# Optimization experiments

Measured on AMD Instinct MI355X. Metric: run time of the kernel, lower is better.

Reference implementation:

```python
import jax, jax.numpy as jnp
import numpy as np

N_HEAD = 16
N_KV_HEAD = 4
HEAD_DIM = 128
N_EMBD = 2048
ROPE_BASE = 100000.0
EPS = 1e-6
MASK_VAL = -10000.0


def _rope_tables(t, dtype):
    half = HEAD_DIM // 2
    inv_freq = 1.0 / (ROPE_BASE ** (jnp.arange(half, dtype=jnp.float32) / half))
    freqs = jnp.arange(t, dtype=jnp.float32)[:, None] * inv_freq[None, :]  # [t, half]
    return jnp.cos(freqs).astype(dtype), jnp.sin(freqs).astype(dtype)


def _apply_rope(x, cos, sin):
    # x: [b, t, h, d]; cos/sin: [t, d//2]
    x1, x2 = jnp.split(x, 2, axis=-1)
    c = cos[None, :, None, :]
    s = sin[None, :, None, :]
    return jnp.concatenate([x1 * c + x2 * s, -x1 * s + x2 * c], axis=-1)


def _rms_norm(x):
    return x * jax.lax.rsqrt(jnp.mean(jnp.square(x), axis=-1, keepdims=True) + EPS)


def setup_inputs() -> dict:
    key = jax.random.key(0)
    ks = jax.random.split(key, 5)
    b, t = 2, 2048
    std = 0.02
    return {
        "x": jax.random.normal(ks[0], (b, t, N_EMBD), dtype=jnp.float32),
        "wq": jax.random.normal(ks[1], (N_EMBD, N_HEAD * HEAD_DIM), dtype=jnp.float32) * std,
        "wk": jax.random.normal(ks[2], (N_EMBD, N_KV_HEAD * HEAD_DIM), dtype=jnp.float32) * std,
        "wv": jax.random.normal(ks[3], (N_EMBD, N_KV_HEAD * HEAD_DIM), dtype=jnp.float32) * std,
        "wo": jax.random.normal(ks[4], (N_EMBD, N_EMBD), dtype=jnp.float32) * std,
    }


def reference(x, wq, wk, wv, wo):
    b, t, _ = x.shape
    group = N_HEAD // N_KV_HEAD

    q = (x @ wq).reshape(b, t, N_HEAD, HEAD_DIM)
    k = (x @ wk).reshape(b, t, N_KV_HEAD, HEAD_DIM)
    v = (x @ wv).reshape(b, t, N_KV_HEAD, HEAD_DIM)

    cos, sin = _rope_tables(t, x.dtype)
    q = _rms_norm(_apply_rope(q, cos, sin))
    k = _rms_norm(_apply_rope(k, cos, sin))

    # GQA expand: [b,t,kvh,d] -> [b,t,h,d]
    k = jnp.repeat(k, group, axis=2)
    v = jnp.repeat(v, group, axis=2)

    scale = jax.lax.rsqrt(jnp.asarray(HEAD_DIM, dtype=q.dtype))
    scores = jnp.einsum("bqhd,bkhd->bhqk", q, k) * scale  # [b,h,t,t]

    causal = jnp.tril(jnp.ones((t, t), dtype=bool))
    scores = jnp.where(causal[None, None, :, :], scores, jnp.asarray(MASK_VAL, scores.dtype))

    probs = jax.nn.softmax(scores.astype(jnp.float32), axis=-1).astype(scores.dtype)

    y = jnp.einsum("bhqk,bkhd->bqhd", probs, v).reshape(b, t, N_EMBD)
    return y @ wo
```

## Files before the change

kernel.cpp:

```cpp
#include <hip/hip_runtime.h>
#include <stdint.h>

typedef unsigned short u16;
typedef unsigned int   u32;
typedef float f32x4  __attribute__((ext_vector_type(4)));
typedef float f32x16 __attribute__((ext_vector_type(16)));
typedef short s16x8  __attribute__((ext_vector_type(8)));

#define T_SEQ 2048
#define NE    2048
#define NH    16
#define NKV   4
#define HD    128
#define QKVW  3072

__device__ __forceinline__ u16 f2bf(float f){
  u32 u = __float_as_uint(f);
  u32 r = u + 0x7FFFu + ((u >> 16) & 1u);
  return (u16)(r >> 16);
}
__device__ __forceinline__ float bf2f(u16 h){ return __uint_as_float(((u32)h) << 16); }

__device__ __forceinline__ u32 pkbf(float a, float b){
  u32 r; asm("v_cvt_pk_bf16_f32 %0, %1, %2" : "=v"(r) : "v"(a), "v"(b)); return r;
}

typedef __attribute__((address_space(3))) u32 lds_u32;
typedef __attribute__((address_space(1))) u32 glb_u32;
__device__ __forceinline__ void g2lds16(const void* g, void* l){
  __builtin_amdgcn_global_load_lds((const glb_u32*)g, (lds_u32*)l, 16, 0, 0);
}

#define PREP_NBLK 18944
__global__ __launch_bounds__(256) void k_prep(const float* __restrict__ x,
                                              const float* __restrict__ wq, const float* __restrict__ wk,
                                              const float* __restrict__ wv, const float* __restrict__ wo,
                                              u16* __restrict__ xb, u16* __restrict__ wqkvT, u16* __restrict__ woT,
                                              float* __restrict__ cosT, float* __restrict__ sinT){
  __shared__ float t[32][33];
  const int blk = blockIdx.x, tid = threadIdx.x;
  if (blk < 8192){
    int i = (blk * 256 + tid) * 4;
    float4 v = *(const float4*)(x + i);
    ushort4 o; o.x = f2bf(v.x); o.y = f2bf(v.y); o.z = f2bf(v.z); o.w = f2bf(v.w);
    *(ushort4*)(xb + i) = o;
    return;
  }
  if (blk >= 18432){
    int i = (blk - 18432) * 256 + tid;
    int tt = i >> 6, j = i & 63;
    float inv = expf(-(float)j * (11.512925464970229f / 64.0f));
    float f = (float)tt * inv;
    cosT[i] = cosf(f);
    sinT[i] = sinf(f);
    return;
  }
  const float* in; u16* out; int C; int tt;
  if      (blk < 12288){ in = wq; out = wqkvT;                     C = 2048; tt = blk - 8192;  }
  else if (blk < 13312){ in = wk; out = wqkvT + (size_t)2048*2048; C = 512;  tt = blk - 12288; }
  else if (blk < 14336){ in = wv; out = wqkvT + (size_t)2560*2048; C = 512;  tt = blk - 13312; }
  else                 { in = wo; out = woT;                       C = 2048; tt = blk - 14336; }
  const int r0 = (tt & 63) * 32, c0 = (tt >> 6) * 32;
  const int tx = tid & 31, ty = tid >> 5;
  #pragma unroll
  for (int i = 0; i < 4; ++i) t[ty + i*8][tx] = in[(size_t)(r0 + ty + i*8) * C + c0 + tx];
  __syncthreads();
  #pragma unroll
  for (int i = 0; i < 4; ++i) out[(size_t)(c0 + ty + i*8) * 2048 + r0 + tx] = f2bf(t[tx][ty + i*8]);
}

#define POST_NBLK 22528
__global__ __launch_bounds__(256) void k_post(u16* __restrict__ qkv, u16* __restrict__ vtb,
                                              const float* __restrict__ cosT, const float* __restrict__ sinT,
                                              float qscale){
  __shared__ u16 tsh[32][33];
  const int blk = blockIdx.x, tid = threadIdx.x;
  if (blk < 20480){
    u16* base; int log2h; float scale; int rh;
    if (blk < 16384){ base = qkv;        log2h = 4; scale = qscale; rh = blk * 4 + (tid >> 6); }
    else            { base = qkv + 2048; log2h = 2; scale = 1.0f;   rh = (blk - 16384) * 4 + (tid >> 6); }
    const int lane = tid & 63;
    const int row = rh >> log2h;
    const int h   = rh & ((1 << log2h) - 1);
    const int t   = row & (T_SEQ - 1);
    u16* p = base + (size_t)row * QKVW + h * HD;
    float x1 = bf2f(p[lane]), x2 = bf2f(p[lane + 64]);
    float c = cosT[t * 64 + lane], s = sinT[t * 64 + lane];
    float y1 = x1 * c + x2 * s;
    float y2 = x2 * c - x1 * s;
    float sq = y1 * y1 + y2 * y2;
    #pragma unroll
    for (int off = 32; off; off >>= 1) sq += __shfl_xor(sq, off);
    float sc = rsqrtf(sq * (1.0f / 128.0f) + 1e-6f) * scale;
    p[lane]      = f2bf(y1 * sc);
    p[lane + 64] = f2bf(y2 * sc);
    return;
  }
  const int tt = blk - 20480;
  const int r0 = (tt & 63) * 32, c0 = ((tt >> 6) & 15) * 32, b = tt >> 10;
  const u16* ib = qkv + (size_t)b * T_SEQ * QKVW + 2560;
  u16*       ob = vtb + (size_t)b * 512 * T_SEQ;
  const int tx = tid & 31, ty = tid >> 5;
  #pragma unroll
  for (int i = 0; i < 4; ++i) tsh[ty + i*8][tx] = ib[(size_t)(r0 + ty + i*8) * QKVW + c0 + tx];
  __syncthreads();
  #pragma unroll
  for (int i = 0; i < 4; ++i) ob[(size_t)(c0 + ty + i*8) * T_SEQ + r0 + tx] = tsh[tx][ty + i*8];
}

__device__ __forceinline__ void cstore(u16* C, size_t i, float v){ C[i] = f2bf(v); }
__device__ __forceinline__ void cstore(float* C, size_t i, float v){ C[i] = v; }

__device__ __forceinline__ void stage_half(const u16* __restrict__ G, int row0, int K, int k0,
                                           u16* lds, int w, int lane){
  #pragma unroll
  for (int call = 0; call < 2; ++call){
    const int o  = call * 256 + w * 64 + lane;
    const int rp = o >> 3, sl = o & 7;
    const int lg = sl ^ (rp & 7);
    const int row = rp * 2 + (lg >> 2);
    const int kc  = lg & 3;
    g2lds16(G + (size_t)(row0 + row) * K + k0 + kc * 8, lds + (size_t)(call * 256 + w * 64) * 8);
  }
}

__device__ __forceinline__ s16x8 ldsFrag(const u16* slotBase, int row, int kchunk){
  const int byte = (row >> 1) * 128 + (((((row & 1) << 2) | kchunk) ^ ((row >> 1) & 7)) << 4);
  return *(const s16x8*)((const char*)slotBase + byte);
}

template <typename CT>
__global__ __launch_bounds__(256, 3) void k_gemm(const u16* __restrict__ A, const u16* __restrict__ BT,
                                                 CT* __restrict__ C, int M, int N, int K, int NPX){
  __shared__ u16 As[3 * 4096];
  __shared__ u16 Bs[3 * 4096];
  const int tid  = threadIdx.x;
  const int lane = tid & 63;
  const int w    = tid >> 6;
  const int wr = w >> 1, wc = w & 1;
  const int bid = blockIdx.x;
  const int xcd = bid & 7, ii = bid >> 3;
  const int ntile = xcd * NPX + ii % NPX;
  const int mtile = ii / NPX;
  const int tm0 = mtile * 128, tn0 = ntile * 128;
  const int frow = lane & 15, fk = lane >> 4;

  f32x4 acc[4][4] = {};
  const int nkt = K >> 6;

  stage_half(A,  tm0, K, 0,  As,        w, lane);
  stage_half(BT, tn0, K, 0,  Bs,        w, lane);
  stage_half(A,  tm0, K, 32, As + 4096, w, lane);
  stage_half(BT, tn0, K, 32, Bs + 4096, w, lane);
  asm volatile("s_waitcnt vmcnt(4)" ::: "memory");
  __builtin_amdgcn_s_barrier();

  int s = 0;
  #pragma unroll 1
  for (int t = 0; t < nkt; ++t){
    const int s1 = (s + 1 > 2) ? 0 : s + 1;
    const int s2 = (s + 2 > 2) ? s - 1 : s + 2;
    const bool more = (t + 1 < nkt);

    if (more){
      stage_half(A,  tm0, K, (t + 1) * 64,  As + s2 * 4096, w, lane);
      stage_half(BT, tn0, K, (t + 1) * 64,  Bs + s2 * 4096, w, lane);
    }
    {
      const u16* Ap = As + s * 4096;
      const u16* Bp = Bs + s * 4096;
      s16x8 af[4], bfr[4];
      #pragma unroll
      for (int m = 0; m < 4; ++m) af[m]  = ldsFrag(Ap, wr * 64 + m * 16 + frow, fk);
      #pragma unroll
      for (int n = 0; n < 4; ++n) bfr[n] = ldsFrag(Bp, wc * 64 + n * 16 + frow, fk);
      __builtin_amdgcn_s_setprio(1);
      #pragma unroll
      for (int m = 0; m < 4; ++m)
        #pragma unroll
        for (int n = 0; n < 4; ++n)
          acc[m][n] = __builtin_amdgcn_mfma_f32_16x16x32_bf16(af[m], bfr[n], acc[m][n], 0, 0, 0);
      __builtin_amdgcn_s_setprio(0);
    }
    if (more) asm volatile("s_waitcnt vmcnt(4)" ::: "memory");
    else      asm volatile("s_waitcnt vmcnt(0)" ::: "memory");
    __builtin_amdgcn_s_barrier();

    if (more){
      stage_half(A,  tm0, K, (t + 1) * 64 + 32, As + s * 4096, w, lane);
      stage_half(BT, tn0, K, (t + 1) * 64 + 32, Bs + s * 4096, w, lane);
    }
    {
      const u16* Ap = As + s1 * 4096;
      const u16* Bp = Bs + s1 * 4096;
      s16x8 af[4], bfr[4];
      #pragma unroll
      for (int m = 0; m < 4; ++m) af[m]  = ldsFrag(Ap, wr * 64 + m * 16 + frow, fk);
      #pragma unroll
      for (int n = 0; n < 4; ++n) bfr[n] = ldsFrag(Bp, wc * 64 + n * 16 + frow, fk);
      __builtin_amdgcn_s_setprio(1);
      #pragma unroll
      for (int m = 0; m < 4; ++m)
        #pragma unroll
        for (int n = 0; n < 4; ++n)
          acc[m][n] = __builtin_amdgcn_mfma_f32_16x16x32_bf16(af[m], bfr[n], acc[m][n], 0, 0, 0);
      __builtin_amdgcn_s_setprio(0);
    }
    if (more){
      asm volatile("s_waitcnt vmcnt(4)" ::: "memory");
      __builtin_amdgcn_s_barrier();
    }
    s = s2;
  }

  #pragma unroll
  for (int m = 0; m < 4; ++m){
    const int row0 = tm0 + wr * 64 + m * 16 + ((lane >> 4) << 2);
    #pragma unroll
    for (int n = 0; n < 4; ++n){
      const int col = tn0 + wc * 64 + n * 16 + (lane & 15);
      #pragma unroll
      for (int r = 0; r < 4; ++r)
        cstore(C, (size_t)(row0 + r) * N + col, acc[m][n][r]);
    }
  }
}

__device__ __forceinline__ s16x8 ldsK(const u16* base, int row, int colB){
  int a = row * 256 + colB; a ^= (row & 7) << 4;
  return *(const s16x8*)((const char*)base + a);
}
__device__ __forceinline__ s16x8 ldsV(const u16* base, int row, int colB){
  int a = row * 128 + colB; a ^= (row & 7) << 4;
  return *(const s16x8*)((const char*)base + a);
}

__global__ __launch_bounds__(256, 2) void k_attn(const u16* __restrict__ qkv, const u16* __restrict__ vt,
                                                 u16* __restrict__ yb){
  __shared__ u16 Kt[2][64 * 128];
  __shared__ u16 Vt[2][128 * 64];
  const int tid = threadIdx.x, lane = tid & 63, w = tid >> 6;
  const int ql = lane & 31, hi = lane >> 5;

  const int bx  = blockIdx.x;
  const int xcd = bx & 7;
  const int b   = xcd >> 2;
  const int kvh = xcd & 3;
  const int slot = bx >> 3;
  const int hl  = slot >> 4;
  const int p   = (slot + 5 * hl) & 15;
  const int h   = kvh * 4 + hl;

  const int tile = (w < 2) ? (31 - p) : p;
  const int tq0  = tile * 64 + (w & 1) * 32;
  const int myq  = tq0 + ql;
  const int nkb  = 32 - p;

  const u16* kg  = qkv + (size_t)(b * T_SEQ) * QKVW + 2048 + kvh * 128;
  const u16* vgb = vt + ((size_t)(b * 512 + kvh * 128)) * T_SEQ;

  auto stageK = [&](int kbI, u16* dst){
    const int ks = kbI * 64;
    #pragma unroll
    for (int cc = 0; cc < 4; ++cc){
      const int call = w * 4 + cc;
      const int o = call * 64 + lane;
      const int f = o ^ ((o >> 4) & 7);
      g2lds16(kg + (size_t)(ks + (o >> 4)) * QKVW + (f & 15) * 8, dst + call * 512);
    }
  };
  auto stageV = [&](int kbI, u16* dst){
    const int ks = kbI * 64;
    #pragma unroll
    for (int cc = 0; cc < 4; ++cc){
      const int call = w * 4 + cc;
      const int o = call * 64 + lane;
      const int f = o ^ ((o >> 3) & 7);
      g2lds16(vgb + (size_t)(o >> 3) * T_SEQ + ks + (f & 7) * 8, dst + call * 512);
    }
  };

  stageK(0, Kt[0]);
  stageV(0, Vt[0]);

  const u16* qrow = qkv + ((size_t)(b * T_SEQ + myq)) * QKVW + h * HD + hi * 8;
  s16x8 qf[8];
  #pragma unroll
  for (int kc = 0; kc < 8; ++kc) qf[kc] = *(const s16x8*)(qrow + kc * 16);

  f32x16 O[4] = {};
  float mloc = -1e30f, lloc = 0.0f;

  asm volatile("s_waitcnt vmcnt(0)" ::: "memory");
  __builtin_amdgcn_s_barrier();

  for (int kbI = 0; kbI < nkb; ++kbI){
    const int ks  = kbI * 64;
    const int cur = kbI & 1;

    if (kbI + 1 < nkb){
      stageV(kbI + 1, Vt[cur ^ 1]);
      stageK(kbI + 1, Kt[cur ^ 1]);
    }

    if (ks <= tq0 + 31){
      const u16* Kc = Kt[cur];
      const u16* Vc = Vt[cur];
      const bool doN1 = (ks + 32 <= tq0 + 31);
      f32x16 S0 = {}, S1 = {};
      __builtin_amdgcn_s_setprio(1);
      #pragma unroll
      for (int kc = 0; kc < 8; ++kc)
        S0 = __builtin_amdgcn_mfma_f32_32x32x16_bf16(ldsK(Kc, ql, kc*32 + hi*16), qf[kc], S0, 0, 0, 0);
      if (doN1){
        #pragma unroll
        for (int kc = 0; kc < 8; ++kc)
          S1 = __builtin_amdgcn_mfma_f32_32x32x16_bf16(ldsK(Kc, 32 + ql, kc*32 + hi*16), qf[kc], S1, 0, 0, 0);
      }
      __builtin_amdgcn_s_setprio(0);
      if (ks + 31 > tq0){
        #pragma unroll
        for (int r = 0; r < 16; ++r)
          if (ks + (r&3) + 8*(r>>2) + 4*hi > myq) S0[r] = -1e30f;
      }
      if (doN1 && (ks + 63 > tq0)){
        #pragma unroll
        for (int r = 0; r < 16; ++r)
          if (ks + 32 + (r&3) + 8*(r>>2) + 4*hi > myq) S1[r] = -1e30f;
      }
      float mr = -1e30f;
      #pragma unroll
      for (int r = 0; r < 16; ++r) mr = fmaxf(mr, S0[r]);
      if (doN1){
        #pragma unroll
        for (int r = 0; r < 16; ++r) mr = fmaxf(mr, S1[r]);
      }
      mr = fmaxf(mr, __shfl_xor(mr, 32));
      if (!__all(mr <= mloc + 8.0f)){
        const float mn = fmaxf(mloc, mr);
        const float a  = __expf(mloc - mn);
        mloc = mn; lloc *= a;
        #pragma unroll
        for (int dt = 0; dt < 4; ++dt)
          #pragma unroll
          for (int r = 0; r < 16; ++r) O[dt][r] *= a;
      }
      float rs = 0.0f;
      #pragma unroll
      for (int r = 0; r < 16; ++r){ S0[r] = __expf(S0[r] - mloc); rs += S0[r]; }
      if (doN1){
        #pragma unroll
        for (int r = 0; r < 16; ++r){ S1[r] = __expf(S1[r] - mloc); rs += S1[r]; }
      }
      rs += __shfl_xor(rs, 32);
      lloc += rs;
      u32 bw[16];
      {
        u32 pk[8], pp[8];
        #pragma unroll
        for (int j = 0; j < 8; ++j) pk[j] = pkbf(S0[2*j], S0[2*j+1]);
        #pragma unroll
        for (int j = 0; j < 8; ++j) pp[j] = (u32)__shfl_xor((int)pk[j], 32);
        bw[0] = hi ? pp[2] : pk[0];  bw[1] = hi ? pp[3] : pk[1];
        bw[2] = hi ? pk[2] : pp[0];  bw[3] = hi ? pk[3] : pp[1];
        bw[4] = hi ? pp[6] : pk[4];  bw[5] = hi ? pp[7] : pk[5];
        bw[6] = hi ? pk[6] : pp[4];  bw[7] = hi ? pk[7] : pp[5];
      }
      int nkc = 2;
      if (doN1){
        u32 pk[8], pp[8];
        #pragma unroll
        for (int j = 0; j < 8; ++j) pk[j] = pkbf(S1[2*j], S1[2*j+1]);
        #pragma unroll
        for (int j = 0; j < 8; ++j) pp[j] = (u32)__shfl_xor((int)pk[j], 32);
        bw[8]  = hi ? pp[2] : pk[0];  bw[9]  = hi ? pp[3] : pk[1];
        bw[10] = hi ? pk[2] : pp[0];  bw[11] = hi ? pk[3] : pp[1];
        bw[12] = hi ? pp[6] : pk[4];  bw[13] = hi ? pp[7] : pk[5];
        bw[14] = hi ? pk[6] : pp[4];  bw[15] = hi ? pk[7] : pp[5];
        nkc = 4;
      }
      __builtin_amdgcn_s_setprio(1);
      #pragma unroll
      for (int kc = 0; kc < 4; ++kc){
        if (kc < nkc){
          union { u32 u[4]; s16x8 v; } pb;
          pb.u[0] = bw[kc*4+0]; pb.u[1] = bw[kc*4+1]; pb.u[2] = bw[kc*4+2]; pb.u[3] = bw[kc*4+3];
          #pragma unroll
          for (int dt = 0; dt < 4; ++dt)
            O[dt] = __builtin_amdgcn_mfma_f32_32x32x16_bf16(ldsV(Vc, dt*32 + ql, kc*32 + hi*16), pb.v, O[dt], 0, 0, 0);
        }
      }
      __builtin_amdgcn_s_setprio(0);
    }

    asm volatile("s_waitcnt vmcnt(0)" ::: "memory");
    __builtin_amdgcn_s_barrier();
  }

  const float linv = 1.0f / lloc;
  u16* yr = yb + ((size_t)(b * T_SEQ + myq)) * NE + h * HD;
  #pragma unroll
  for (int dt = 0; dt < 4; ++dt){
    #pragma unroll
    for (int mq = 0; mq < 4; ++mq){
      uint2 s;
      s.x = pkbf(O[dt][4*mq+0] * linv, O[dt][4*mq+1] * linv);
      s.y = pkbf(O[dt][4*mq+2] * linv, O[dt][4*mq+3] * linv);
      *(uint2*)(yr + dt*32 + 8*mq + 4*hi) = s;
    }
  }
}

extern "C" void kernel_launch(void* const* d_in, const int* in_sizes, int n_in,
                              void* d_out, int out_size, void* d_ws, size_t ws_size,
                              hipStream_t stream){
  const float* x  = (const float*)d_in[0];
  const float* wq = (const float*)d_in[1];
  const float* wk = (const float*)d_in[2];
  const float* wv = (const float*)d_in[3];
  const float* wo = (const float*)d_in[4];
  float* out = (float*)d_out;

  char* w = (char*)d_ws;
  u16* xb    = (u16*)w;  w += (size_t)4096 * 2048 * 2;
  u16* wqkvT = (u16*)w;  w += (size_t)3072 * 2048 * 2;
  u16* woT   = (u16*)w;  w += (size_t)2048 * 2048 * 2;
  u16* qkv   = (u16*)w;  w += (size_t)4096 * 3072 * 2;
  u16* vtb   = (u16*)w;  w += (size_t)4096 * 512  * 2;
  u16* yb    = (u16*)w;  w += (size_t)4096 * 2048 * 2;
  float* cosT = (float*)w; w += (size_t)2048 * 64 * 4;
  float* sinT = (float*)w; w += (size_t)2048 * 64 * 4;

  const float SCALE = 0.08838834764831845f;

  k_prep<<<PREP_NBLK, 256, 0, stream>>>(x, wq, wk, wv, wo, xb, wqkvT, woT, cosT, sinT);

  k_gemm<u16><<<768, 256, 0, stream>>>(xb, wqkvT, qkv, 4096, QKVW, 2048, 3);

  k_post<<<POST_NBLK, 256, 0, stream>>>(qkv, vtb, cosT, sinT, SCALE);

  k_attn<<<512, 256, 0, stream>>>(qkv, vtb, yb);

  k_gemm<float><<<512, 256, 0, stream>>>(yb, woT, out, 4096, 2048, 2048, 2);
}
```

Measured before the change: 220.9 us.

## Widen GEMM tiles to 128x256 with per-wave 128x64 subtiles and remap blocks

The GEMM kernel's block tile grows from 128x128 to 128x256. Each of the four waves now computes a 128x64 strip, holding 8x4 accumulators, and the B staging buffer is doubled. The block-to-tile mapping is also changed so that the four consecutive m-tiles on an XCD share a B column tile, and the grid size is halved for both GEMMs. This raises arithmetic intensity per LDS load and improves L2 reuse, at the cost of more registers (occupancy hint drops from 3 to 2) and fewer blocks, which for the 256-block output GEMM means at most one wave of blocks over the CUs.

```diff
diff --git a/kernel.cpp b/kernel.cpp
--- a/kernel.cpp
+++ b/kernel.cpp
@@ -111,10 +111,11 @@
 __device__ __forceinline__ void cstore(u16* C, size_t i, float v){ C[i] = f2bf(v); }
 __device__ __forceinline__ void cstore(float* C, size_t i, float v){ C[i] = v; }
 
+template <int NCALL>
 __device__ __forceinline__ void stage_half(const u16* __restrict__ G, int row0, int K, int k0,
                                            u16* lds, int w, int lane){
   #pragma unroll
-  for (int call = 0; call < 2; ++call){
+  for (int call = 0; call < NCALL; ++call){
     const int o  = call * 256 + w * 64 + lane;
     const int rp = o >> 3, sl = o & 7;
     const int lg = sl ^ (rp & 7);
@@ -130,29 +131,28 @@
 }
 
 template <typename CT>
-__global__ __launch_bounds__(256, 3) void k_gemm(const u16* __restrict__ A, const u16* __restrict__ BT,
-                                                 CT* __restrict__ C, int M, int N, int K, int NPX){
+__global__ __launch_bounds__(256, 2) void k_gemm(const u16* __restrict__ A, const u16* __restrict__ BT,
+                                                 CT* __restrict__ C, int M, int N, int K){
   __shared__ u16 As[3 * 4096];
-  __shared__ u16 Bs[3 * 4096];
+  __shared__ u16 Bs[3 * 8192];
   const int tid  = threadIdx.x;
   const int lane = tid & 63;
   const int w    = tid >> 6;
-  const int wr = w >> 1, wc = w & 1;
   const int bid = blockIdx.x;
   const int xcd = bid & 7, ii = bid >> 3;
-  const int ntile = xcd * NPX + ii % NPX;
-  const int mtile = ii / NPX;
-  const int tm0 = mtile * 128, tn0 = ntile * 128;
+  const int mtile = xcd * 4 + (ii & 3);
+  const int ntile = ii >> 2;
+  const int tm0 = mtile * 128, tn0 = ntile * 256;
   const int frow = lane & 15, fk = lane >> 4;
 
-  f32x4 acc[4][4] = {};
+  f32x4 acc[8][4] = {};
   const int nkt = K >> 6;
 
-  stage_half(A,  tm0, K, 0,  As,        w, lane);
-  stage_half(BT, tn0, K, 0,  Bs,        w, lane);
-  stage_half(A,  tm0, K, 32, As + 4096, w, lane);
-  stage_half(BT, tn0, K, 32, Bs + 4096, w, lane);
-  asm volatile("s_waitcnt vmcnt(4)" ::: "memory");
+  stage_half<2>(A,  tm0, K, 0,  As,        w, lane);
+  stage_half<4>(BT, tn0, K, 0,  Bs,        w, lane);
+  stage_half<2>(A,  tm0, K, 32, As + 4096, w, lane);
+  stage_half<4>(BT, tn0, K, 32, Bs + 8192, w, lane);
+  asm volatile("s_waitcnt vmcnt(6)" ::: "memory");
   __builtin_amdgcn_s_barrier();
 
   int s = 0;
@@ -163,62 +163,62 @@
     const bool more = (t + 1 < nkt);
 
     if (more){
-      stage_half(A,  tm0, K, (t + 1) * 64,  As + s2 * 4096, w, lane);
-      stage_half(BT, tn0, K, (t + 1) * 64,  Bs + s2 * 4096, w, lane);
+      stage_half<2>(A,  tm0, K, (t + 1) * 64,  As + s2 * 4096, w, lane);
+      stage_half<4>(BT, tn0, K, (t + 1) * 64,  Bs + s2 * 8192, w, lane);
     }
     {
       const u16* Ap = As + s * 4096;
-      const u16* Bp = Bs + s * 4096;
-      s16x8 af[4], bfr[4];
-      #pragma unroll
-      for (int m = 0; m < 4; ++m) af[m]  = ldsFrag(Ap, wr * 64 + m * 16 + frow, fk);
-      #pragma unroll
-      for (int n = 0; n < 4; ++n) bfr[n] = ldsFrag(Bp, wc * 64 + n * 16 + frow, fk);
+      const u16* Bp = Bs + s * 8192;
+      s16x8 af[8], bfr[4];
+      #pragma unroll
+      for (int m = 0; m < 8; ++m) af[m]  = ldsFrag(Ap, m * 16 + frow, fk);
+      #pragma unroll
+      for (int n = 0; n < 4; ++n) bfr[n] = ldsFrag(Bp, w * 64 + n * 16 + frow, fk);
       __builtin_amdgcn_s_setprio(1);
       #pragma unroll
-      for (int m = 0; m < 4; ++m)
+      for (int m = 0; m < 8; ++m)
         #pragma unroll
         for (int n = 0; n < 4; ++n)
           acc[m][n] = __builtin_amdgcn_mfma_f32_16x16x32_bf16(af[m], bfr[n], acc[m][n], 0, 0, 0);
       __builtin_amdgcn_s_setprio(0);
     }
-    if (more) asm volatile("s_waitcnt vmcnt(4)" ::: "memory");
+    if (more) asm volatile("s_waitcnt vmcnt(6)" ::: "memory");
     else      asm volatile("s_waitcnt vmcnt(0)" ::: "memory");
     __builtin_amdgcn_s_barrier();
 
     if (more){
-      stage_half(A,  tm0, K, (t + 1) * 64 + 32, As + s * 4096, w, lane);
-      stage_half(BT, tn0, K, (t + 1) * 64 + 32, Bs + s * 4096, w, lane);
+      stage_half<2>(A,  tm0, K, (t + 1) * 64 + 32, As + s * 4096, w, lane);
+      stage_half<4>(BT, tn0, K, (t + 1) * 64 + 32, Bs + s * 8192, w, lane);
     }
     {
       const u16* Ap = As + s1 * 4096;
-      const u16* Bp = Bs + s1 * 4096;
-      s16x8 af[4], bfr[4];
-      #pragma unroll
-      for (int m = 0; m < 4; ++m) af[m]  = ldsFrag(Ap, wr * 64 + m * 16 + frow, fk);
-      #pragma unroll
-      for (int n = 0; n < 4; ++n) bfr[n] = ldsFrag(Bp, wc * 64 + n * 16 + frow, fk);
+      const u16* Bp = Bs + s1 * 8192;
+      s16x8 af[8], bfr[4];
+      #pragma unroll
+      for (int m = 0; m < 8; ++m) af[m]  = ldsFrag(Ap, m * 16 + frow, fk);
+      #pragma unroll
+      for (int n = 0; n < 4; ++n) bfr[n] = ldsFrag(Bp, w * 64 + n * 16 + frow, fk);
       __builtin_amdgcn_s_setprio(1);
       #pragma unroll
-      for (int m = 0; m < 4; ++m)
+      for (int m = 0; m < 8; ++m)
         #pragma unroll
         for (int n = 0; n < 4; ++n)
           acc[m][n] = __builtin_amdgcn_mfma_f32_16x16x32_bf16(af[m], bfr[n], acc[m][n], 0, 0, 0);
       __builtin_amdgcn_s_setprio(0);
     }
     if (more){
-      asm volatile("s_waitcnt vmcnt(4)" ::: "memory");
+      asm volatile("s_waitcnt vmcnt(6)" ::: "memory");
       __builtin_amdgcn_s_barrier();
     }
     s = s2;
   }
 
   #pragma unroll
-  for (int m = 0; m < 4; ++m){
-    const int row0 = tm0 + wr * 64 + m * 16 + ((lane >> 4) << 2);
+  for (int m = 0; m < 8; ++m){
+    const int row0 = tm0 + m * 16 + ((lane >> 4) << 2);
     #pragma unroll
     for (int n = 0; n < 4; ++n){
-      const int col = tn0 + wc * 64 + n * 16 + (lane & 15);
+      const int col = tn0 + w * 64 + n * 16 + (lane & 15);
       #pragma unroll
       for (int r = 0; r < 4; ++r)
         cstore(C, (size_t)(row0 + r) * N + col, acc[m][n][r]);
@@ -435,11 +435,11 @@
 
   k_prep<<<PREP_NBLK, 256, 0, stream>>>(x, wq, wk, wv, wo, xb, wqkvT, woT, cosT, sinT);
 
-  k_gemm<u16><<<768, 256, 0, stream>>>(xb, wqkvT, qkv, 4096, QKVW, 2048, 3);
+  k_gemm<u16><<<384, 256, 0, stream>>>(xb, wqkvT, qkv, 4096, QKVW, 2048);
 
   k_post<<<POST_NBLK, 256, 0, stream>>>(qkv, vtb, cosT, sinT, SCALE);
 
   k_attn<<<512, 256, 0, stream>>>(qkv, vtb, yb);
 
-  k_gemm<float><<<512, 256, 0, stream>>>(yb, woT, out, 4096, 2048, 2048, 2);
-}
+  k_gemm<float><<<256, 256, 0, stream>>>(yb, woT, out, 4096, 2048, 2048);
+}
```

Result: slower. 240.9 us (+9.0%).
